# Performance work log

Hardware: AMD Instinct MI355X
Metric: run time of the kernel (lower is better)

Reference implementation:

```python
import jax, jax.numpy as jnp
import numpy as np

NUM_CLASSES = 250
NUM_EMB = 128
EMB_DIM = 512
HID = 256
IN_DIM = 225
COMMIT = 0.25


def _lstm_dir(x, Wih, Whh, b, reverse):
    # x: [B, T, D]; Wih: [4H, D]; Whh: [4H, H]; b: [4H]
    B = x.shape[0]
    H = Whh.shape[1]
    xs = jnp.swapaxes(x, 0, 1)            # [T, B, D]
    pre = xs @ Wih.T + b                   # precompute input projection: [T, B, 4H]

    def step(carry, pre_t):
        h, c = carry
        g = pre_t + h @ Whh.T
        i, f, gg, o = jnp.split(g, 4, axis=-1)  # torch gate order i,f,g,o
        i = jax.nn.sigmoid(i)
        f = jax.nn.sigmoid(f)
        gg = jnp.tanh(gg)
        o = jax.nn.sigmoid(o)
        c = f * c + i * gg
        h = o * jnp.tanh(c)
        return (h, c), h

    init = (jnp.zeros((B, H), x.dtype), jnp.zeros((B, H), x.dtype))
    _, hs = jax.lax.scan(step, init, pre, reverse=reverse)
    return jnp.swapaxes(hs, 0, 1)          # [B, T, H]


def _bilstm(x, Wih_f, Whh_f, b_f, Wih_b, Whh_b, b_b):
    hf = _lstm_dir(x, Wih_f, Whh_f, b_f, reverse=False)
    hb = _lstm_dir(x, Wih_b, Whh_b, b_b, reverse=True)
    return jnp.concatenate([hf, hb], axis=-1)  # [B, T, 2H]


def _vq(z, codebook):
    flat = z.reshape(-1, codebook.shape[1])  # [N, E]
    d = (jnp.sum(flat ** 2, axis=1, keepdims=True)
         + jnp.sum(codebook ** 2, axis=1)
         - 2.0 * flat @ codebook.T)          # [N, K]
    idx = jnp.argmin(d, axis=1)              # [N]
    q = codebook[idx].reshape(z.shape)
    e_loss = jnp.mean((jax.lax.stop_gradient(q) - z) ** 2)
    q_loss = jnp.mean((q - jax.lax.stop_gradient(z)) ** 2)
    loss = q_loss + COMMIT * e_loss
    q_st = z + jax.lax.stop_gradient(q - z)  # straight-through
    return q_st, loss


def setup_inputs() -> dict:
    key = jax.random.key(0)
    ks = jax.random.split(key, 16)
    s = 0.05
    d = {
        'x': jax.random.normal(ks[0], (64, 512, IN_DIM), dtype=jnp.float32),
        'enc_Wih_f': jax.random.normal(ks[1], (4 * HID, IN_DIM), jnp.float32) * s,
        'enc_Whh_f': jax.random.normal(ks[2], (4 * HID, HID), jnp.float32) * s,
        'enc_b_f': jnp.zeros((4 * HID,), jnp.float32),
        'enc_Wih_b': jax.random.normal(ks[3], (4 * HID, IN_DIM), jnp.float32) * s,
        'enc_Whh_b': jax.random.normal(ks[4], (4 * HID, HID), jnp.float32) * s,
        'enc_b_b': jnp.zeros((4 * HID,), jnp.float32),
        'codebook': jax.random.uniform(ks[5], (NUM_EMB, EMB_DIM), jnp.float32,
                                       minval=-1.0 / NUM_EMB, maxval=1.0 / NUM_EMB),
        'dec_Wih_f': jax.random.normal(ks[6], (4 * HID, EMB_DIM), jnp.float32) * s,
        'dec_Whh_f': jax.random.normal(ks[7], (4 * HID, HID), jnp.float32) * s,
        'dec_b_f': jnp.zeros((4 * HID,), jnp.float32),
        'dec_Wih_b': jax.random.normal(ks[8], (4 * HID, EMB_DIM), jnp.float32) * s,
        'dec_Whh_b': jax.random.normal(ks[9], (4 * HID, HID), jnp.float32) * s,
        'dec_b_b': jnp.zeros((4 * HID,), jnp.float32),
        'W_cls': jax.random.normal(ks[10], (NUM_CLASSES, EMB_DIM), jnp.float32) * s,
        'b_cls': jnp.zeros((NUM_CLASSES,), jnp.float32),
    }
    return d


def reference(x, enc_Wih_f, enc_Whh_f, enc_b_f, enc_Wih_b, enc_Whh_b, enc_b_b,
              codebook, dec_Wih_f, dec_Whh_f, dec_b_f, dec_Wih_b, dec_Whh_b, dec_b_b,
              W_cls, b_cls):
    enc_out = _bilstm(x, enc_Wih_f, enc_Whh_f, enc_b_f, enc_Wih_b, enc_Whh_b, enc_b_b)  # [B,T,512]
    quantized, vq_loss = _vq(enc_out, codebook)
    dec_out = _bilstm(quantized, dec_Wih_f, dec_Whh_f, dec_b_f, dec_Wih_b, dec_Whh_b, dec_b_b)
    logits = dec_out[:, -1] @ W_cls.T + b_cls  # [B, num_classes]
    return logits, vq_loss
```

## Files before the change

kernel.cpp:

```cpp
#include <hip/hip_runtime.h>
#include <hip/hip_fp16.h>
#include <cstddef>

#define Bb 64
#define Tt 512
#define INRAW 225
#define Hh 256
#define G4 1024
#define Ee 512
#define NCODE 128
#define NCLS 250

typedef _Float16 half8_t __attribute__((ext_vector_type(8)));
typedef float f32x4 __attribute__((ext_vector_type(4)));

__device__ __forceinline__ float sigf(float x) { return 1.0f / (1.0f + expf(-x)); }
__device__ __forceinline__ float fsig(float x) { return __builtin_amdgcn_rcpf(1.0f + __expf(-x)); }
__device__ __forceinline__ float ftanh(float x) {
  return 2.0f * __builtin_amdgcn_rcpf(1.0f + __expf(-2.0f * x)) - 1.0f;
}

__device__ __forceinline__ unsigned pkmax16(unsigned a, unsigned b) {
  unsigned r;
  asm("v_pk_max_i16 %0, %1, %2" : "=v"(r) : "v"(a), "v"(b));
  return r;
}

__global__ __launch_bounds__(256) void fill_inf_k(unsigned* __restrict__ p, long n) {
  long i = (long)blockIdx.x * 256 + threadIdx.x;
  const long stride = (long)gridDim.x * 256;
  unsigned v = 0x7C007C00u;
  for (; i < n; i += stride) {
    asm volatile("global_store_dword %0, %1, off sc0 sc1" :: "v"(p + i), "v"(v) : "memory");
  }
}

__global__ __launch_bounds__(256) void conv_x_h(const float* __restrict__ src,
                                                _Float16* __restrict__ dst) {
  int idx = blockIdx.x * 256 + threadIdx.x;
  int row = idx >> 8, k = idx & 255;
  dst[idx] = (k < INRAW) ? (_Float16)src[(size_t)row * INRAW + k] : (_Float16)0.f;
}

__global__ __launch_bounds__(256) void pack_w_k(const float* __restrict__ W,
                                                float* __restrict__ wp, int K) {
  int idx = blockIdx.x * 256 + threadIdx.x;
  int jg = idx / K;
  if (jg >= 1024) return;
  int k = idx - jg * K;
  int j = jg >> 2, g = jg & 3;
  wp[(((size_t)k << 8) + j) * 4 + g] = W[(size_t)(g * 256 + j) * K + k];
}

__global__ __launch_bounds__(256) void pack_w_frag(const float* __restrict__ W,
                                                   _Float16* __restrict__ wp) {
  int idx = blockIdx.x * 256 + threadIdx.x;
  int e = idx & 7, l = (idx >> 3) & 63, zg = (idx >> 9) & 7;
  int ks = (idx >> 12) & 7, wv = (idx >> 15) & 7;
  int z = zg >> 2, g = zg & 3;
  int u = wv * 32 + z * 16 + (l & 15);
  int k = ks * 32 + (l >> 4) * 8 + e;
  wp[idx] = (_Float16)W[(size_t)(g * 256 + u) * 256 + k];
}

__global__ __launch_bounds__(256) void pack_wih_frag(const float* __restrict__ W,
                                                     _Float16* __restrict__ wp,
                                                     int Kraw, int ksbits) {
  int idx = blockIdx.x * 256 + threadIdx.x;
  int KS = 1 << ksbits;
  int e = idx & 7, l = (idx >> 3) & 63;
  int tail = idx >> 9;
  int ks = tail & (KS - 1); tail >>= ksbits;
  int z = tail & 1, w = (tail >> 1) & 7, g = tail >> 4;
  if (g >= 4) return;
  int k = ks * 32 + (l >> 4) * 8 + e;
  int u = w * 32 + z * 16 + (l & 15);
  wp[idx] = (k < Kraw) ? (_Float16)W[(size_t)(g * 256 + u) * Kraw + k] : (_Float16)0.f;
}

__global__ __launch_bounds__(256) void gemm_mfma_pre(const _Float16* __restrict__ Ah,
                                                     const _Float16* __restrict__ Bp,
                                                     const float* __restrict__ bias,
                                                     __half* __restrict__ C, int K) {
  const int t = blockIdx.x, g = blockIdx.y;
  const int bg = threadIdx.x >> 6;
  const int l = threadIdx.x & 63, l15 = l & 15, lg = l >> 4;
  const int KS = K >> 5;

  f32x4 acc[16];
#pragma unroll
  for (int ct = 0; ct < 16; ++ct) acc[ct] = (f32x4){0.f, 0.f, 0.f, 0.f};

  const _Float16* arow = Ah + ((size_t)(bg * 16 + l15) * 512 + t) * K + lg * 8;

  for (int kh = 0; kh < KS; kh += 8) {
    half8_t af[8];
#pragma unroll
    for (int k2 = 0; k2 < 8; ++k2)
      af[k2] = *(const half8_t*)(arow + (kh + k2) * 32);
#pragma unroll
    for (int ct = 0; ct < 16; ++ct) {
      const int w = ct >> 1, z = ct & 1;
      const _Float16* bb = Bp + ((((size_t)(g * 8 + w) * 2 + z) * KS + kh) * 64 + l) * 8;
#pragma unroll
      for (int k2 = 0; k2 < 8; ++k2) {
        half8_t bf = *(const half8_t*)(bb + (size_t)k2 * 512);
        acc[ct] = __builtin_amdgcn_mfma_f32_16x16x32_f16(af[k2], bf, acc[ct], 0, 0, 0);
      }
    }
  }

#pragma unroll
  for (int ct = 0; ct < 16; ++ct) {
    const int w = ct >> 1, z = ct & 1;
    const int u = w * 32 + z * 16 + l15;
    const float bs = bias[g * 256 + u];
    union { unsigned short us[4]; uint2 u2; } pk;
#pragma unroll
    for (int j = 0; j < 4; ++j) {
      __half hv = __float2half(acc[ct][j] + bs);
      pk.us[j] = *(unsigned short*)&hv;
    }
    __half* dst = C + ((((size_t)t * 4 + bg) * 8 + w) * 2 + z) * 1024 + l * 16 + g * 4;
    *(uint2*)dst = pk.u2;
  }
}

__global__ __launch_bounds__(64) void lstm_scan_sync(
    const half8_t* __restrict__ preF, const half8_t* __restrict__ wF,
    _Float16* __restrict__ hexF,
    const half8_t* __restrict__ preB, const half8_t* __restrict__ wB,
    _Float16* __restrict__ hexB, int nfwd) {
  const int isB = (blockIdx.x >= nfwd) ? 1 : 0;
  const half8_t* pre = isB ? preB : preF;
  const half8_t* wfrag = isB ? wB : wF;
  _Float16* hex = isB ? hexB : hexF;
  const int bid = blockIdx.x - (isB ? nfwd : 0);
  const int rg = bid >> 4, sl = bid & 15;
  const int w_ = sl >> 1, z_ = sl & 1;
  const int l = threadIdx.x, l15 = l & 15, lg = l >> 4;
  const int u0 = sl * 16;

  half8_t bfr[8][4];
#pragma unroll
  for (int ks = 0; ks < 8; ++ks)
#pragma unroll
    for (int g = 0; g < 4; ++g)
      bfr[ks][g] = wfrag[(size_t)((w_ * 8 + ks) * 8 + z_ * 4 + g) * 64 + l];

  float c[4] = {0.f, 0.f, 0.f, 0.f};
  half8_t pc0, pc1;
  {
    const int t0 = isB ? (Tt - 1) : 0;
    const half8_t* pp = pre + ((size_t)(t0 * 4 + rg) * 16 + sl) * 128 + l * 2;
    pc0 = pp[0]; pc1 = pp[1];
  }

  for (int s = 0; s < Tt; ++s) {
    f32x4 acc[4];
#pragma unroll
    for (int g = 0; g < 4; ++g)
#pragma unroll
      for (int j = 0; j < 4; ++j)
        acc[g][j] = (float)((g < 2 ? pc0 : pc1)[(g & 1) * 4 + j]);

    if (s + 1 < Tt) {
      const int tn = isB ? (Tt - 2 - s) : (s + 1);
      const half8_t* pp = pre + ((size_t)(tn * 4 + rg) * 16 + sl) * 128 + l * 2;
      pc0 = pp[0]; pc1 = pp[1];
    }

    if (s > 0) {
      const char* ab = (const char*)hex + (((size_t)(s - 1) * 64 + rg * 16) * 256) * 2;
      half8_t afr[8];
      while (true) {
#pragma unroll
        for (int ks = 0; ks < 8; ++ks) {
          const void* ap = (const void*)(ab + l15 * 512 + ks * 64 + lg * 16);
          asm volatile("global_load_dwordx4 %0, %1, off sc0 sc1"
                       : "=v"(afr[ks]) : "v"(ap) : "memory");
        }
        asm volatile("s_waitcnt vmcnt(0)" ::: "memory");
        union HU { half8_t h; uint4 u; } cu;
        cu.h = afr[0];
        unsigned mm = pkmax16(pkmax16(cu.u.x, cu.u.y), pkmax16(cu.u.z, cu.u.w));
#pragma unroll
        for (int ks = 1; ks < 8; ++ks) {
          cu.h = afr[ks];
          mm = pkmax16(mm, pkmax16(pkmax16(cu.u.x, cu.u.y), pkmax16(cu.u.z, cu.u.w)));
        }
        int bad = ((mm & 0xFFFFu) == 0x7C00u) || ((mm >> 16) == 0x7C00u);
        if (__all(!bad)) break;
      }
      __builtin_amdgcn_sched_barrier(0);

#pragma unroll
      for (int ks = 0; ks < 8; ++ks)
#pragma unroll
        for (int g = 0; g < 4; ++g)
          acc[g] = __builtin_amdgcn_mfma_f32_16x16x32_f16(afr[ks], bfr[ks][g], acc[g], 0, 0, 0);
    }

#pragma unroll
    for (int j = 0; j < 4; ++j) {
      float iv = fsig(acc[0][j]);
      float fv = fsig(acc[1][j]);
      float gv = ftanh(acc[2][j]);
      float ov = fsig(acc[3][j]);
      c[j] = fv * c[j] + iv * gv;
      float hv = ov * ftanh(c[j]);
      union { _Float16 f; unsigned short u; } cv;
      cv.f = (_Float16)hv;
      unsigned hb32 = cv.u;
      const void* hp = (const void*)(hex + ((size_t)s * 64 + rg * 16 + lg * 4 + j) * 256
                                     + u0 + l15);
      asm volatile("global_store_short %0, %1, off sc0 sc1"
                   :: "v"(hp), "v"(hb32) : "memory");
    }
  }
}

#define VPB 4
__global__ __launch_bounds__(128) void vq_kernel(const _Float16* __restrict__ hexF,
                                                 const _Float16* __restrict__ hexB,
                                                 const float* __restrict__ cb,
                                                 _Float16* __restrict__ qh,
                                                 float* __restrict__ dmin) {
  const int tid = threadIdx.x;
  const int v0 = blockIdx.x * VPB;
  __shared__ __align__(16) float zs[VPB][Ee];
  __shared__ float dsh[NCODE];
  __shared__ int ish[NCODE];
  __shared__ int best[VPB];

#pragma unroll
  for (int v = 0; v < VPB; ++v) {
    const int vv = v0 + v;
    const int b = vv >> 9, t = vv & 511;
    const _Float16* hf = hexF + ((size_t)t * 64 + b) * 256;
    const _Float16* hb = hexB + ((size_t)(Tt - 1 - t) * 64 + b) * 256;
    zs[v][tid]       = (float)hf[tid];
    zs[v][tid + 128] = (float)hf[tid + 128];
    zs[v][tid + 256] = (float)hb[tid];
    zs[v][tid + 384] = (float)hb[tid + 128];
  }
  __syncthreads();

  float dv[VPB] = {0.0f, 0.0f, 0.0f, 0.0f};
  const float4* crow = (const float4*)(cb + (size_t)tid * Ee);
#pragma unroll 2
  for (int e4 = 0; e4 < Ee / 4; ++e4) {
    float4 cc = crow[e4];
#pragma unroll
    for (int v = 0; v < VPB; ++v) {
      float4 z = *(const float4*)&zs[v][e4 * 4];
      float t0 = z.x - cc.x, t1 = z.y - cc.y, t2 = z.z - cc.z, t3 = z.w - cc.w;
      dv[v] = fmaf(t0, t0, dv[v]);
      dv[v] = fmaf(t1, t1, dv[v]);
      dv[v] = fmaf(t2, t2, dv[v]);
      dv[v] = fmaf(t3, t3, dv[v]);
    }
  }

#pragma unroll
  for (int v = 0; v < VPB; ++v) {
    __syncthreads();
    dsh[tid] = dv[v];
    ish[tid] = tid;
    __syncthreads();
    for (int off = 64; off > 0; off >>= 1) {
      if (tid < off) {
        float dn = dsh[tid + off];
        int in_ = ish[tid + off];
        if (dn < dsh[tid] || (dn == dsh[tid] && in_ < ish[tid])) {
          dsh[tid] = dn;
          ish[tid] = in_;
        }
      }
      __syncthreads();
    }
    if (tid == 0) {
      best[v] = ish[0];
      dmin[v0 + v] = dsh[0];
    }
  }
  __syncthreads();

#pragma unroll
  for (int v = 0; v < VPB; ++v) {
    const float* cbest = cb + (size_t)best[v] * Ee;
    _Float16* qrow = qh + (size_t)(v0 + v) * Ee;
#pragma unroll
    for (int u = 0; u < 4; ++u) {
      int e = tid + u * 128;
      float z = zs[v][e];
      qrow[e] = (_Float16)(z + (cbest[e] - z));
    }
  }
}

__global__ __launch_bounds__(256) void vq_reduce(const float* __restrict__ dmin,
                                                 float* __restrict__ out) {
  __shared__ float sh[256];
  int tid = threadIdx.x;
  float s = 0.0f;
  for (int i = tid; i < Bb * Tt; i += 256) s += dmin[i];
  sh[tid] = s;
  __syncthreads();
  for (int off = 128; off > 0; off >>= 1) {
    if (tid < off) sh[tid] += sh[tid + off];
    __syncthreads();
  }
  if (tid == 0) out[Bb * NCLS] = sh[0] * (1.25f / ((float)(Bb * Tt) * (float)Ee));
}

__global__ __launch_bounds__(256) void dec_bwd_last(const _Float16* __restrict__ qh,
                                                    const float* __restrict__ wpB,
                                                    const float* __restrict__ bias,
                                                    float* __restrict__ hb_last) {
  int b = blockIdx.x, tid = threadIdx.x;
  __shared__ __align__(16) float zsl[Ee];
  const _Float16* qrow = qh + ((size_t)b * Tt + (Tt - 1)) * Ee;
  zsl[tid] = (float)qrow[tid];
  zsl[tid + 256] = (float)qrow[tid + 256];
  __syncthreads();
  float a0 = bias[tid], a1 = bias[256 + tid], a2 = bias[512 + tid], a3 = bias[768 + tid];
  const float4* wp4 = (const float4*)wpB;
#pragma unroll 4
  for (int k = 0; k < Ee; ++k) {
    float zk = zsl[k];
    float4 w = wp4[((size_t)k << 8) + tid];
    a0 = fmaf(zk, w.x, a0); a1 = fmaf(zk, w.y, a1);
    a2 = fmaf(zk, w.z, a2); a3 = fmaf(zk, w.w, a3);
  }
  float i = sigf(a0), f = sigf(a1), g = tanhf(a2), o = sigf(a3);
  (void)f;
  float cc = i * g;
  hb_last[b * Hh + tid] = o * tanhf(cc);
}

__global__ __launch_bounds__(256) void classifier_k(const _Float16* __restrict__ hexD,
                                                    const float* __restrict__ hb_last,
                                                    const float* __restrict__ Wcls,
                                                    const float* __restrict__ bcls,
                                                    float* __restrict__ out) {
  int b = blockIdx.x, tid = threadIdx.x;
  __shared__ __align__(16) float dl[Ee];
  dl[tid] = (float)hexD[((size_t)(Tt - 1) * 64 + b) * 256 + tid];
  dl[tid + 256] = hb_last[b * Hh + tid];
  __syncthreads();
  if (tid < NCLS) {
    const float4* wr = (const float4*)(Wcls + (size_t)tid * Ee);
    float acc = bcls[tid];
#pragma unroll 4
    for (int e4 = 0; e4 < Ee / 4; ++e4) {
      float4 w = wr[e4];
      float4 z = *(const float4*)&dl[e4 * 4];
      acc = fmaf(w.x, z.x, acc);
      acc = fmaf(w.y, z.y, acc);
      acc = fmaf(w.z, z.z, acc);
      acc = fmaf(w.w, z.w, acc);
    }
    out[b * NCLS + tid] = acc;
  }
}

extern "C" void kernel_launch(void* const* d_in, const int* in_sizes, int n_in,
                              void* d_out, int out_size, void* d_ws, size_t ws_size,
                              hipStream_t stream) {
  const float* x     = (const float*)d_in[0];
  const float* eWihF = (const float*)d_in[1];
  const float* eWhhF = (const float*)d_in[2];
  const float* ebF   = (const float*)d_in[3];
  const float* eWihB = (const float*)d_in[4];
  const float* eWhhB = (const float*)d_in[5];
  const float* ebB   = (const float*)d_in[6];
  const float* cb    = (const float*)d_in[7];
  const float* dWihF = (const float*)d_in[8];
  const float* dWhhF = (const float*)d_in[9];
  const float* dbF   = (const float*)d_in[10];
  const float* dWihB = (const float*)d_in[11];
  const float* dbB   = (const float*)d_in[13];
  const float* Wcls  = (const float*)d_in[14];
  const float* bcls  = (const float*)d_in[15];
  float* out = (float*)d_out;
  float* w = (float*)d_ws;

  const size_t MR = (size_t)Bb * Tt;
  const size_t SZ_PRE_H = MR * G4 / 2;
  const size_t SZ_HEX  = (size_t)Tt * Bb * Hh / 2;
  const size_t SZ_XH   = MR * 256 / 2;
  const size_t SZ_WPK  = (size_t)512 * G4;
  const size_t SZ_WPH  = (size_t)G4 * Hh / 2;
  const size_t SZ_WIH  = (size_t)4 * 8 * 2 * 8 * 64 * 8 / 2;
  const size_t SZ_WIHD = SZ_WIH * 2;

  size_t o = 0;
  __half* preFh = (__half*)(w + o); o += SZ_PRE_H;
  __half* preBh = (__half*)(w + o); o += SZ_PRE_H;
  _Float16* hexF = (_Float16*)(w + o); o += SZ_HEX;
  _Float16* hexB = (_Float16*)(w + o); o += SZ_HEX;
  _Float16* hexD = (_Float16*)(w + o); o += SZ_HEX;
  _Float16* xh = (_Float16*)(w + o); o += SZ_XH;
  float* wpkbd = w + o; o += SZ_WPK;
  _Float16* wphF = (_Float16*)(w + o); o += SZ_WPH;
  _Float16* wphB = (_Float16*)(w + o); o += SZ_WPH;
  _Float16* wphD = (_Float16*)(w + o); o += SZ_WPH;
  _Float16* wpihF = (_Float16*)(w + o); o += SZ_WIH;
  _Float16* wpihB = (_Float16*)(w + o); o += SZ_WIH;
  _Float16* wpihD = (_Float16*)(w + o); o += SZ_WIHD;
  float* dminp = w + o; o += MR;
  float* hbl   = w + o; o += (size_t)Bb * Hh;
  _Float16* qh = (_Float16*)preFh;
  __half* dprf = preBh;

  hipLaunchKernelGGL(fill_inf_k, dim3(2048), dim3(256), 0, stream,
                     (unsigned*)hexF, (long)(3 * SZ_HEX));
  hipLaunchKernelGGL(conv_x_h, dim3((int)(MR * 256 / 256)), dim3(256), 0, stream, x, xh);
  hipLaunchKernelGGL(pack_w_k, dim3((G4 * 512) / 256), dim3(256), 0, stream, dWihB, wpkbd, 512);
  hipLaunchKernelGGL(pack_w_frag, dim3(1024), dim3(256), 0, stream, eWhhF, wphF);
  hipLaunchKernelGGL(pack_w_frag, dim3(1024), dim3(256), 0, stream, eWhhB, wphB);
  hipLaunchKernelGGL(pack_w_frag, dim3(1024), dim3(256), 0, stream, dWhhF, wphD);
  hipLaunchKernelGGL(pack_wih_frag, dim3(1024), dim3(256), 0, stream, eWihF, wpihF, INRAW, 3);
  hipLaunchKernelGGL(pack_wih_frag, dim3(1024), dim3(256), 0, stream, eWihB, wpihB, INRAW, 3);
  hipLaunchKernelGGL(pack_wih_frag, dim3(2048), dim3(256), 0, stream, dWihF, wpihD, Ee, 4);

  hipLaunchKernelGGL(gemm_mfma_pre, dim3(Tt, 4), dim3(256), 0, stream,
                     xh, wpihF, ebF, preFh, 256);
  hipLaunchKernelGGL(gemm_mfma_pre, dim3(Tt, 4), dim3(256), 0, stream,
                     xh, wpihB, ebB, preBh, 256);

  hipLaunchKernelGGL(lstm_scan_sync, dim3(128), dim3(64), 0, stream,
                     (const half8_t*)preFh, (const half8_t*)wphF, hexF,
                     (const half8_t*)preBh, (const half8_t*)wphB, hexB, 64);

  hipLaunchKernelGGL(vq_kernel, dim3((int)(MR / VPB)), dim3(128), 0, stream,
                     hexF, hexB, cb, qh, dminp);
  hipLaunchKernelGGL(vq_reduce, dim3(1), dim3(256), 0, stream, dminp, out);

  hipLaunchKernelGGL(gemm_mfma_pre, dim3(Tt, 4), dim3(256), 0, stream,
                     qh, wpihD, dbF, dprf, 512);

  hipLaunchKernelGGL(dec_bwd_last, dim3(Bb), dim3(256), 0, stream, qh, wpkbd, dbB, hbl);

  hipLaunchKernelGGL(lstm_scan_sync, dim3(64), dim3(64), 0, stream,
                     (const half8_t*)dprf, (const half8_t*)wphD, hexD,
                     (const half8_t*)dprf, (const half8_t*)wphD, hexD, 64);

  hipLaunchKernelGGL(classifier_k, dim3(Bb), dim3(256), 0, stream,
                     hexD, hbl, Wcls, bcls, out);
}
```

Before: 2.574 ms.

## Pair LSTM scan slices into 8-wave blocks sharing half of h via LDS

```diff
diff --git a/kernel.cpp b/kernel.cpp
--- a/kernel.cpp
+++ b/kernel.cpp
@@ -13,6 +13,7 @@
 
 typedef _Float16 half8_t __attribute__((ext_vector_type(8)));
 typedef float f32x4 __attribute__((ext_vector_type(4)));
+typedef unsigned u32x4 __attribute__((ext_vector_type(4)));
 
 __device__ __forceinline__ float sigf(float x) { return 1.0f / (1.0f + expf(-x)); }
 __device__ __forceinline__ float fsig(float x) { return __builtin_amdgcn_rcpf(1.0f + __expf(-x)); }
@@ -26,12 +27,12 @@
   return r;
 }
 
-__global__ __launch_bounds__(256) void fill_inf_k(unsigned* __restrict__ p, long n) {
+__global__ __launch_bounds__(256) void fill_inf4_k(u32x4* __restrict__ p, long n4) {
   long i = (long)blockIdx.x * 256 + threadIdx.x;
   const long stride = (long)gridDim.x * 256;
-  unsigned v = 0x7C007C00u;
-  for (; i < n; i += stride) {
-    asm volatile("global_store_dword %0, %1, off sc0 sc1" :: "v"(p + i), "v"(v) : "memory");
+  u32x4 v = {0x7C007C00u, 0x7C007C00u, 0x7C007C00u, 0x7C007C00u};
+  for (; i < n4; i += stride) {
+    asm volatile("global_store_dwordx4 %0, %1, off sc0 sc1" :: "v"(p + i), "v"(v) : "memory");
   }
 }
 
@@ -126,20 +127,23 @@
   }
 }
 
-__global__ __launch_bounds__(64) void lstm_scan_sync(
-    const half8_t* __restrict__ preF, const half8_t* __restrict__ wF,
-    _Float16* __restrict__ hexF,
+__global__ __launch_bounds__(512, 1) void lstm_scan_pair(
+    const half8_t* __restrict__ preA, const half8_t* __restrict__ wA,
+    _Float16* __restrict__ hexA,
     const half8_t* __restrict__ preB, const half8_t* __restrict__ wB,
-    _Float16* __restrict__ hexB, int nfwd) {
-  const int isB = (blockIdx.x >= nfwd) ? 1 : 0;
-  const half8_t* pre = isB ? preB : preF;
-  const half8_t* wfrag = isB ? wB : wF;
-  _Float16* hex = isB ? hexB : hexF;
-  const int bid = blockIdx.x - (isB ? nfwd : 0);
-  const int rg = bid >> 4, sl = bid & 15;
+    _Float16* __restrict__ hexB, int nA) {
+  const int isB = (blockIdx.x >= nA) ? 1 : 0;
+  const half8_t* pre = isB ? preB : preA;
+  const half8_t* wfrag = isB ? wB : wA;
+  _Float16* hex = isB ? hexB : hexA;
+  const int bid = blockIdx.x - (isB ? nA : 0);
+  const int uh = bid & 1, rh = bid >> 1;
+  const int wv = threadIdx.x >> 6;
+  const int l = threadIdx.x & 63, l15 = l & 15, lg = l >> 4;
+  const int sl = uh * 8 + wv;
   const int w_ = sl >> 1, z_ = sl & 1;
-  const int l = threadIdx.x, l15 = l & 15, lg = l >> 4;
-  const int u0 = sl * 16;
+
+  __shared__ __align__(16) char hsh[2][4096];
 
   half8_t bfr[8][4];
 #pragma unroll
@@ -152,10 +156,11 @@
   half8_t pc0, pc1;
   {
     const int t0 = isB ? (Tt - 1) : 0;
-    const half8_t* pp = pre + ((size_t)(t0 * 4 + rg) * 16 + sl) * 128 + l * 2;
+    const half8_t* pp = pre + ((size_t)(t0 * 4 + rh) * 16 + sl) * 128 + l * 2;
     pc0 = pp[0]; pc1 = pp[1];
   }
 
+  int cur = 0;
   for (int s = 0; s < Tt; ++s) {
     f32x4 acc[4];
 #pragma unroll
@@ -166,41 +171,65 @@
 
     if (s + 1 < Tt) {
       const int tn = isB ? (Tt - 2 - s) : (s + 1);
-      const half8_t* pp = pre + ((size_t)(tn * 4 + rg) * 16 + sl) * 128 + l * 2;
+      const half8_t* pp = pre + ((size_t)(tn * 4 + rh) * 16 + sl) * 128 + l * 2;
       pc0 = pp[0]; pc1 = pp[1];
     }
 
     if (s > 0) {
-      const char* ab = (const char*)hex + (((size_t)(s - 1) * 64 + rg * 16) * 256) * 2;
-      half8_t afr[8];
+      const char* ab = (const char*)hex + ((size_t)(s - 1) * 64 + rh * 16) * 512;
+      half8_t afrP[4];
+
+#define ISSUEP()                                                              \
+      do {                                                                    \
+        _Pragma("unroll")                                                     \
+        for (int kk = 0; kk < 4; ++kk) {                                      \
+          const void* ap = (const void*)(ab + l15 * 512 +                     \
+                                         ((1 - uh) * 4 + kk) * 64 + lg * 16); \
+          asm volatile("global_load_dwordx4 %0, %1, off sc0 sc1"              \
+                       : "=v"(afrP[kk]) : "v"(ap) : "memory");                \
+        }                                                                     \
+      } while (0)
+
+      ISSUEP();
+
+      const char* rb = hsh[cur];
+#pragma unroll
+      for (int kk = 0; kk < 4; ++kk) {
+        const int byte = (l15 * 256 + kk * 64 + lg * 16) ^ ((l15 & 7) << 4);
+        half8_t ao = *(const half8_t*)(rb + byte);
+#pragma unroll
+        for (int g = 0; g < 4; ++g)
+          acc[g] = __builtin_amdgcn_mfma_f32_16x16x32_f16(ao, bfr[uh * 4 + kk][g],
+                                                          acc[g], 0, 0, 0);
+      }
+
       while (true) {
-#pragma unroll
-        for (int ks = 0; ks < 8; ++ks) {
-          const void* ap = (const void*)(ab + l15 * 512 + ks * 64 + lg * 16);
-          asm volatile("global_load_dwordx4 %0, %1, off sc0 sc1"
-                       : "=v"(afr[ks]) : "v"(ap) : "memory");
-        }
         asm volatile("s_waitcnt vmcnt(0)" ::: "memory");
-        union HU { half8_t h; uint4 u; } cu;
-        cu.h = afr[0];
-        unsigned mm = pkmax16(pkmax16(cu.u.x, cu.u.y), pkmax16(cu.u.z, cu.u.w));
-#pragma unroll
-        for (int ks = 1; ks < 8; ++ks) {
-          cu.h = afr[ks];
-          mm = pkmax16(mm, pkmax16(pkmax16(cu.u.x, cu.u.y), pkmax16(cu.u.z, cu.u.w)));
+        __builtin_amdgcn_sched_barrier(0);
+        union HU { half8_t h; u32x4 u; } cu;
+        cu.h = afrP[0];
+        unsigned mm = pkmax16(pkmax16(cu.u[0], cu.u[1]), pkmax16(cu.u[2], cu.u[3]));
+#pragma unroll
+        for (int kk = 1; kk < 4; ++kk) {
+          cu.h = afrP[kk];
+          mm = pkmax16(mm, pkmax16(pkmax16(cu.u[0], cu.u[1]), pkmax16(cu.u[2], cu.u[3])));
         }
         int bad = ((mm & 0xFFFFu) == 0x7C00u) || ((mm >> 16) == 0x7C00u);
         if (__all(!bad)) break;
+        ISSUEP();
       }
       __builtin_amdgcn_sched_barrier(0);
 
 #pragma unroll
-      for (int ks = 0; ks < 8; ++ks)
+      for (int kk = 0; kk < 4; ++kk)
 #pragma unroll
         for (int g = 0; g < 4; ++g)
-          acc[g] = __builtin_amdgcn_mfma_f32_16x16x32_f16(afr[ks], bfr[ks][g], acc[g], 0, 0, 0);
-    }
-
+          acc[g] = __builtin_amdgcn_mfma_f32_16x16x32_f16(
+              afrP[kk], bfr[(1 - uh) * 4 + kk][g], acc[g], 0, 0, 0);
+#undef ISSUEP
+    }
+
+    char* wb = hsh[cur ^ 1];
 #pragma unroll
     for (int j = 0; j < 4; ++j) {
       float iv = fsig(acc[0][j]);
@@ -209,14 +238,19 @@
       float ov = fsig(acc[3][j]);
       c[j] = fv * c[j] + iv * gv;
       float hv = ov * ftanh(c[j]);
+      const int rloc = lg * 4 + j;
+      const int wbyte = (rloc * 256 + (wv * 16 + l15) * 2) ^ ((rloc & 7) << 4);
       union { _Float16 f; unsigned short u; } cv;
       cv.f = (_Float16)hv;
+      *(_Float16*)(wb + wbyte) = cv.f;
       unsigned hb32 = cv.u;
-      const void* hp = (const void*)(hex + ((size_t)s * 64 + rg * 16 + lg * 4 + j) * 256
-                                     + u0 + l15);
+      const void* hp = (const void*)(hex + ((size_t)s * 64 + rh * 16 + rloc) * 256
+                                     + uh * 128 + wv * 16 + l15);
       asm volatile("global_store_short %0, %1, off sc0 sc1"
                    :: "v"(hp), "v"(hb32) : "memory");
     }
+    __syncthreads();
+    cur ^= 1;
   }
 }
 
@@ -414,8 +448,8 @@
   _Float16* qh = (_Float16*)preFh;
   __half* dprf = preBh;
 
-  hipLaunchKernelGGL(fill_inf_k, dim3(2048), dim3(256), 0, stream,
-                     (unsigned*)hexF, (long)(3 * SZ_HEX));
+  hipLaunchKernelGGL(fill_inf4_k, dim3(2048), dim3(256), 0, stream,
+                     (u32x4*)hexF, (long)(3 * SZ_HEX / 4));
   hipLaunchKernelGGL(conv_x_h, dim3((int)(MR * 256 / 256)), dim3(256), 0, stream, x, xh);
   hipLaunchKernelGGL(pack_w_k, dim3((G4 * 512) / 256), dim3(256), 0, stream, dWihB, wpkbd, 512);
   hipLaunchKernelGGL(pack_w_frag, dim3(1024), dim3(256), 0, stream, eWhhF, wphF);
@@ -430,9 +464,9 @@
   hipLaunchKernelGGL(gemm_mfma_pre, dim3(Tt, 4), dim3(256), 0, stream,
                      xh, wpihB, ebB, preBh, 256);
 
-  hipLaunchKernelGGL(lstm_scan_sync, dim3(128), dim3(64), 0, stream,
+  hipLaunchKernelGGL(lstm_scan_pair, dim3(16), dim3(512), 0, stream,
                      (const half8_t*)preFh, (const half8_t*)wphF, hexF,
-                     (const half8_t*)preBh, (const half8_t*)wphB, hexB, 64);
+                     (const half8_t*)preBh, (const half8_t*)wphB, hexB, 8);
 
   hipLaunchKernelGGL(vq_kernel, dim3((int)(MR / VPB)), dim3(128), 0, stream,
                      hexF, hexB, cb, qh, dminp);
@@ -443,9 +477,9 @@
 
   hipLaunchKernelGGL(dec_bwd_last, dim3(Bb), dim3(256), 0, stream, qh, wpkbd, dbB, hbl);
 
-  hipLaunchKernelGGL(lstm_scan_sync, dim3(64), dim3(64), 0, stream,
+  hipLaunchKernelGGL(lstm_scan_pair, dim3(8), dim3(512), 0, stream,
                      (const half8_t*)dprf, (const half8_t*)wphD, hexD,
-                     (const half8_t*)dprf, (const half8_t*)wphD, hexD, 64);
+                     (const half8_t*)dprf, (const half8_t*)wphD, hexD, 8);
 
   hipLaunchKernelGGL(classifier_k, dim3(Bb), dim3(256), 0, stream,
                      hexD, hbl, Wcls, bcls, out);
```

After: 10.09 ms. 292% more time.
